# Optimization experiments

Hardware: AMD Instinct MI355X
Metric: run time of the kernel (lower is better)

Reference implementation:

```python
import jax, jax.numpy as jnp
import numpy as np

H = 512
TAU = 5
B = 16384
EPS = 1e-5


def layer_norm(x, gamma, beta):
    mu = jnp.mean(x, axis=-1, keepdims=True)
    var = jnp.var(x, axis=-1, keepdims=True)
    return (x - mu) * jax.lax.rsqrt(var + EPS) * gamma + beta


def setup_inputs() -> dict:
    key = jax.random.key(0)
    ks = jax.random.split(key, 12)
    s = 1.0 / np.sqrt(H)
    inp = {
        "T_t": jax.random.normal(ks[0], (B, H), jnp.float32),
        "S_t": jax.random.normal(ks[1], (B, H), jnp.float32),
        "t_att": jax.random.normal(ks[2], (TAU, B, H), jnp.float32),
        "s_att": jax.random.normal(ks[3], (TAU, B, H), jnp.float32),
        # Lin_t_next: in_features(H) -> H, + LayerNorm
        "W_tn": jax.random.uniform(ks[4], (H, H), jnp.float32, -s, s),
        "b_tn": jnp.zeros((H,), jnp.float32),
        "g_tn": jnp.ones((H,), jnp.float32),
        "be_tn": jnp.zeros((H,), jnp.float32),
        # Lin_s_next: H -> H, + LayerNorm
        "W_sn": jax.random.uniform(ks[5], (H, H), jnp.float32, -s, s),
        "b_sn": jnp.zeros((H,), jnp.float32),
        "g_sn": jnp.ones((H,), jnp.float32),
        "be_sn": jnp.zeros((H,), jnp.float32),
        # Lin_t: H -> 3H, + LayerNorm
        "W_t": jax.random.uniform(ks[6], (H, 3 * H), jnp.float32, -s, s),
        "b_t": jnp.zeros((3 * H,), jnp.float32),
        "g_t": jnp.ones((3 * H,), jnp.float32),
        "be_t": jnp.zeros((3 * H,), jnp.float32),
        # Lin_s: H -> 3H, + LayerNorm
        "W_s": jax.random.uniform(ks[7], (H, 3 * H), jnp.float32, -s, s),
        "b_s": jnp.zeros((3 * H,), jnp.float32),
        "g_s": jnp.ones((3 * H,), jnp.float32),
        "be_s": jnp.zeros((3 * H,), jnp.float32),
    }
    return inp


def reference(T_t, S_t, t_att, s_att,
              W_tn, b_tn, g_tn, be_tn,
              W_sn, b_sn, g_sn, be_sn,
              W_t, b_t, g_t, be_t,
              W_s, b_s, g_s, be_s):
    s_next = layer_norm(S_t @ W_sn + b_sn, g_sn, be_sn)        # [B,H]
    t_next = layer_norm(T_t @ W_tn + b_tn, g_tn, be_tn)        # [B,H]

    # attention weights over tau trend steps
    scale = 1.0 / jnp.sqrt(jnp.asarray(H, T_t.dtype))
    weights = jnp.einsum('tbh,bh->tb', s_att, s_next) * scale   # [tau,B]
    weights = jax.nn.softmax(weights, axis=0)[..., None]        # [tau,B,1]
    T_trend = jnp.sum(t_att * weights, axis=0)                  # [B,H]

    t_att_gate = jax.nn.sigmoid(t_next)
    T_fusion = T_t * t_att_gate + (1.0 - t_att_gate) * T_trend

    T_concat = layer_norm(T_fusion @ W_t + b_t, g_t, be_t)      # [B,3H]
    S_concat = layer_norm(S_t @ W_s + b_s, g_s, be_s)           # [B,3H]
    t_g, t_t, t_s = jnp.split(T_concat, 3, axis=1)
    s_g, s_t, s_s = jnp.split(S_concat, 3, axis=1)

    T_gate = jax.nn.sigmoid(t_g)
    S_gate = jax.nn.sigmoid(s_g)
    T_new = T_gate * t_t + (1.0 - T_gate) * s_t
    S_new = S_gate * s_s + (1.0 - S_gate) * t_s
    S_new = S_new + S_t  # cell_mode == 'residual'
    return (T_new, S_new)
```

## Files before the change

kernel.cpp:

```cpp
#include <hip/hip_runtime.h>

#define Bsz 16384
#define Hd  512
#define TAUn 5
#define EPSv 1e-5f

typedef short bf16x8 __attribute__((ext_vector_type(8)));
typedef float f32x4  __attribute__((ext_vector_type(4)));

__device__ __forceinline__ float bf2f(short s) {
    union { unsigned u; float f; } v;
    v.u = ((unsigned)(unsigned short)s) << 16;
    return v.f;
}
__device__ __forceinline__ short f2bf(float f) {
    union { float f; unsigned u; } v; v.f = f;
    unsigned r = v.u + 0x7fffu + ((v.u >> 16) & 1u);
    return (short)(r >> 16);
}
__device__ __forceinline__ float sigm(float x) {
    return 1.0f / (1.0f + expf(-x));
}

__device__ __forceinline__ void gload16(const void* gsrc, void* lds) {
    __builtin_amdgcn_global_load_lds(
        (const __attribute__((address_space(1))) void*)gsrc,
        (__attribute__((address_space(3))) void*)lds, 16, 0, 0);
}

__device__ __forceinline__ float load1(const void* p, size_t i, int isbf) {
    return isbf ? bf2f(((const short*)p)[i]) : ((const float*)p)[i];
}
__device__ __forceinline__ void load8f(const void* p, size_t off, int isbf, float o[8]) {
    if (isbf) {
        bf16x8 v = *(const bf16x8*)((const short*)p + off);
#pragma unroll
        for (int j = 0; j < 8; ++j) o[j] = bf2f(v[j]);
    } else {
        const float* f = (const float*)p + off;
        float4 a = *(const float4*)f, b = *(const float4*)(f + 4);
        o[0]=a.x; o[1]=a.y; o[2]=a.z; o[3]=a.w; o[4]=b.x; o[5]=b.y; o[6]=b.z; o[7]=b.w;
    }
}
__device__ __forceinline__ bf16x8 load8bf(const void* p, size_t off, int isbf) {
    if (isbf) return *(const bf16x8*)((const short*)p + off);
    const float* f = (const float*)p + off;
    bf16x8 r;
#pragma unroll
    for (int j = 0; j < 8; ++j) r[j] = f2bf(f[j]);
    return r;
}

__global__ void detect_dtype(const void* g_tn, int* flag) {
    if (threadIdx.x == 0 && blockIdx.x == 0)
        *flag = (((const unsigned*)g_tn)[0] == 0x3F803F80u) ? 1 : 0;
}

__global__ void transpose_any(const void* __restrict__ in, short* __restrict__ out,
                              int K, int N, const int* __restrict__ flagp) {
    __shared__ short tile[32][33];
    const int isbf = *flagp;
    int n0 = blockIdx.x * 32, k0 = blockIdx.y * 32;
    int tx = threadIdx.x, ty = threadIdx.y;
    for (int i = ty; i < 32; i += 8) {
        size_t idx = (size_t)(k0 + i) * N + n0 + tx;
        tile[i][tx] = isbf ? ((const short*)in)[idx] : f2bf(((const float*)in)[idx]);
    }
    __syncthreads();
    for (int i = ty; i < 32; i += 8)
        out[(size_t)(n0 + i) * K + k0 + tx] = tile[tx][i];
}

__global__ __launch_bounds__(256) void conv_bf16(const void* __restrict__ in,
                                                 short* __restrict__ out,
                                                 const int* __restrict__ flagp) {
    const int isbf = *flagp;
    size_t i = ((size_t)blockIdx.x * 256 + threadIdx.x) * 8;
    *(bf16x8*)(out + i) = load8bf(in, i, isbf);
}

__global__ __launch_bounds__(256) void pack_weights(const void* __restrict__ in,
                                                    short* __restrict__ out,
                                                    int N, const int* __restrict__ flagp) {
    const int isbf = *flagp;
    const int lane = threadIdx.x & 63;
    const int packet = blockIdx.x * 4 + (threadIdx.x >> 6);
    const int nc = packet >> 4;
    const int kc = packet & 15;
    const int n  = nc * 16 + (lane & 15);
    const int kb = kc * 32 + (lane >> 4) * 8;
    bf16x8 v;
#pragma unroll
    for (int j = 0; j < 8; ++j) {
        size_t idx = (size_t)(kb + j) * N + n;
        v[j] = isbf ? ((const short*)in)[idx] : f2bf(((const float*)in)[idx]);
    }
    *(bf16x8*)(out + (size_t)packet * 512 + lane * 8) = v;
}

__global__ __launch_bounds__(256) void gemm128(
    const short* __restrict__ A, const short* __restrict__ BT,
    short* __restrict__ C, int N)
{
    __shared__ short As[2][128 * 32];
    __shared__ short Bs[2][128 * 32];
    const int tid  = threadIdx.x;
    const int wv   = tid >> 6, lane = tid & 63;
    const int m16  = lane & 15, quad = lane >> 4;
    const int mt = blockIdx.x & 127, nt = blockIdx.x >> 7;
    const int m0 = mt * 128, n0 = nt * 128;
    const int wm = wv >> 1, wn = wv & 1;

    f32x4 acc[16];
#pragma unroll
    for (int i = 0; i < 16; ++i) acc[i] = (f32x4){0.f, 0.f, 0.f, 0.f};

    auto STAGE = [&](int buf, int kc) {
        const int k0 = kc * 32;
#pragma unroll
        for (int o = 0; o < 2; ++o) {
            int g = o * 256 + tid;
            int row = g >> 2, unit = g & 3;
            gload16(A  + (size_t)(m0 + row) * Hd + k0 + unit * 8,
                    (short*)As[buf] + (size_t)(o * 256 + wv * 64) * 8);
            gload16(BT + (size_t)(n0 + row) * Hd + k0 + unit * 8,
                    (short*)Bs[buf] + (size_t)(o * 256 + wv * 64) * 8);
        }
    };

    STAGE(0, 0);
    __syncthreads();
    for (int kc = 0; kc < 16; ++kc) {
        const int cur = kc & 1;
        if (kc < 15) STAGE(cur ^ 1, kc + 1);
        bf16x8 a[4], b[4];
#pragma unroll
        for (int f = 0; f < 4; ++f) {
            a[f] = *(const bf16x8*)&As[cur][(wm * 64 + f * 16 + m16) * 32 + quad * 8];
            b[f] = *(const bf16x8*)&Bs[cur][(wn * 64 + f * 16 + m16) * 32 + quad * 8];
        }
#pragma unroll
        for (int fm = 0; fm < 4; ++fm)
#pragma unroll
            for (int fn = 0; fn < 4; ++fn)
                acc[fm * 4 + fn] = __builtin_amdgcn_mfma_f32_16x16x32_bf16(
                    a[fm], b[fn], acc[fm * 4 + fn], 0, 0, 0);
        __syncthreads();
    }

#pragma unroll
    for (int fm = 0; fm < 4; ++fm)
#pragma unroll
        for (int fn = 0; fn < 4; ++fn) {
            int col = n0 + wn * 64 + fn * 16 + m16;
#pragma unroll
            for (int r = 0; r < 4; ++r) {
                int row = m0 + wm * 64 + fm * 16 + quad * 4 + r;
                C[(size_t)row * N + col] = f2bf(acc[fm * 4 + fn][r]);
            }
        }
}

__global__ __launch_bounds__(256) void kernelA2(
    const short* __restrict__ Cs, const short* __restrict__ Ct,
    const void* __restrict__ T_t, const void* __restrict__ t_att, const void* __restrict__ s_att,
    const void* __restrict__ b_tn, const void* __restrict__ g_tn, const void* __restrict__ be_tn,
    const void* __restrict__ b_sn, const void* __restrict__ g_sn, const void* __restrict__ be_sn,
    short* __restrict__ T_fus, const int* __restrict__ flagp)
{
    __shared__ float xs[16][Hd + 4];
    __shared__ float xt[16][Hd + 4];
    __shared__ float red[4][16][16];
    __shared__ float stat[4][16];
    __shared__ float wts[TAUn][16];

    const int isbf = *flagp;
    const int tid  = threadIdx.x;
    const int wave = tid >> 6;
    const int lane = tid & 63;
    const int row0 = blockIdx.x * 16;

    for (int i = 0; i < 4; ++i) {
        int unit = tid + i * 256;
        int r = unit >> 6, c = (unit & 63) * 8;
        bf16x8 vs8 = *(const bf16x8*)(Cs + (size_t)(row0 + r) * Hd + c);
        bf16x8 vt8 = *(const bf16x8*)(Ct + (size_t)(row0 + r) * Hd + c);
#pragma unroll
        for (int j = 0; j < 8; ++j) {
            xs[r][c + j] = bf2f(vs8[j]) + load1(b_sn, c + j, isbf);
            xt[r][c + j] = bf2f(vt8[j]) + load1(b_tn, c + j, isbf);
        }
    }
    __syncthreads();

    {
        int r = tid >> 4, lw = tid & 15;
        float s1 = 0, s2 = 0, t1 = 0, t2 = 0;
        for (int c = lw; c < Hd; c += 16) {
            float v = xs[r][c]; s1 += v; s2 += v * v;
            float u = xt[r][c]; t1 += u; t2 += u * u;
        }
        red[0][r][lw] = s1; red[1][r][lw] = s2; red[2][r][lw] = t1; red[3][r][lw] = t2;
    }
    __syncthreads();
    if (tid < 16) {
        float a = 0, b = 0, c = 0, d = 0;
        for (int i = 0; i < 16; ++i) { a += red[0][tid][i]; b += red[1][tid][i]; c += red[2][tid][i]; d += red[3][tid][i]; }
        float muS = a / Hd, varS = b / Hd - muS * muS;
        float muT = c / Hd, varT = d / Hd - muT * muT;
        stat[0][tid] = muS; stat[1][tid] = rsqrtf(varS + EPSv);
        stat[2][tid] = muT; stat[3][tid] = rsqrtf(varT + EPSv);
    }
    __syncthreads();
    for (int idx = tid; idx < 16 * Hd; idx += 256) {
        int r = idx >> 9, c = idx & (Hd - 1);
        xs[r][c] = (xs[r][c] - stat[0][r]) * stat[1][r] * load1(g_sn, c, isbf) + load1(be_sn, c, isbf);
        xt[r][c] = (xt[r][c] - stat[2][r]) * stat[3][r] * load1(g_tn, c, isbf) + load1(be_tn, c, isbf);
    }
    __syncthreads();

    const float scale = 0.044194173824159216f;
    for (int r2 = 0; r2 < 4; ++r2) {
        int row = wave * 4 + r2;
        size_t b = (size_t)(row0 + row);
        float xsv[8];
#pragma unroll
        for (int j = 0; j < 8; ++j) xsv[j] = xs[row][lane * 8 + j];
        for (int t = 0; t < TAUn; ++t) {
            float sa[8];
            load8f(s_att, ((size_t)t * Bsz + b) * Hd + lane * 8, isbf, sa);
            float p = 0;
#pragma unroll
            for (int j = 0; j < 8; ++j) p += sa[j] * xsv[j];
            for (int off = 32; off > 0; off >>= 1) p += __shfl_xor(p, off);
            if (lane == 0) wts[t][row] = p * scale;
        }
    }
    __syncthreads();
    if (tid < 16) {
        float mx = -1e30f;
        for (int t = 0; t < TAUn; ++t) mx = fmaxf(mx, wts[t][tid]);
        float e[TAUn], s = 0;
        for (int t = 0; t < TAUn; ++t) { e[t] = expf(wts[t][tid] - mx); s += e[t]; }
        for (int t = 0; t < TAUn; ++t) wts[t][tid] = e[t] / s;
    }
    __syncthreads();

    for (int it = 0; it < 4; ++it) {
        int c = tid + it * 256;
        int row = c >> 6, h0 = (c & 63) * 8;
        size_t b = (size_t)(row0 + row);
        float tt[8];
        load8f(T_t, b * Hd + h0, isbf, tt);
        float w[TAUn];
        for (int t = 0; t < TAUn; ++t) w[t] = wts[t][row];
        float ta[TAUn][8];
        for (int t = 0; t < TAUn; ++t)
            load8f(t_att, ((size_t)t * Bsz + b) * Hd + h0, isbf, ta[t]);
        bf16x8 o;
#pragma unroll
        for (int j = 0; j < 8; ++j) {
            float g = sigm(xt[row][h0 + j]);
            float trend = 0;
            for (int t = 0; t < TAUn; ++t) trend += w[t] * ta[t][j];
            o[j] = f2bf(tt[j] * g + (1.f - g) * trend);
        }
        *(bf16x8*)(T_fus + b * Hd + h0) = o;
    }
}

__global__ __launch_bounds__(256) void kernelC2(
    const short* __restrict__ Cu, const short* __restrict__ Cv, const void* __restrict__ S_t,
    const void* __restrict__ b_t, const void* __restrict__ g_t, const void* __restrict__ be_t,
    const void* __restrict__ b_s, const void* __restrict__ g_s, const void* __restrict__ be_s,
    void* __restrict__ out, const int* __restrict__ flagp)
{
    const int isbf = *flagp;
    const int lane = threadIdx.x & 63;
    const size_t row = (size_t)blockIdx.x * 4 + (threadIdx.x >> 6);
    const float n3inv = 1.0f / 1536.0f;

    float u[3][8], v[3][8];
    float su = 0, qu = 0, sv = 0, qv = 0;
#pragma unroll
    for (int k = 0; k < 3; ++k) {
        int c0 = (k * 64 + lane) * 8;
        bf16x8 a = *(const bf16x8*)(Cu + row * 1536 + c0);
        bf16x8 b = *(const bf16x8*)(Cv + row * 1536 + c0);
        float bt[8], bs[8];
        load8f(b_t, c0, isbf, bt);
        load8f(b_s, c0, isbf, bs);
#pragma unroll
        for (int j = 0; j < 8; ++j) {
            float x = bf2f(a[j]) + bt[j];
            float y = bf2f(b[j]) + bs[j];
            u[k][j] = x; v[k][j] = y;
            su += x; qu += x * x; sv += y; qv += y * y;
        }
    }
    for (int mk = 32; mk >= 1; mk >>= 1) {
        su += __shfl_xor(su, mk); qu += __shfl_xor(qu, mk);
        sv += __shfl_xor(sv, mk); qv += __shfl_xor(qv, mk);
    }
    float muU = su * n3inv, rU = rsqrtf(qu * n3inv - muU * muU + EPSv);
    float muV = sv * n3inv, rV = rsqrtf(qv * n3inv - muV * muV + EPSv);

    float guv[3][8], beu[3][8], gvv[3][8], bev[3][8];
#pragma unroll
    for (int k = 0; k < 3; ++k) {
        int c0 = (k * 64 + lane) * 8;
        load8f(g_t,  c0, isbf, guv[k]);
        load8f(be_t, c0, isbf, beu[k]);
        load8f(g_s,  c0, isbf, gvv[k]);
        load8f(be_s, c0, isbf, bev[k]);
    }
    float stv[8];
    load8f(S_t, row * Hd + lane * 8, isbf, stv);

    float Tn[8], Sn[8];
#pragma unroll
    for (int j = 0; j < 8; ++j) {
        float ug = (u[0][j] - muU) * rU * guv[0][j] + beu[0][j];
        float ut = (u[1][j] - muU) * rU * guv[1][j] + beu[1][j];
        float us = (u[2][j] - muU) * rU * guv[2][j] + beu[2][j];
        float vg = (v[0][j] - muV) * rV * gvv[0][j] + bev[0][j];
        float vt = (v[1][j] - muV) * rV * gvv[1][j] + bev[1][j];
        float vs = (v[2][j] - muV) * rV * gvv[2][j] + bev[2][j];
        float Tg = sigm(ug), Sg = sigm(vg);
        Tn[j] = Tg * ut + (1.f - Tg) * vt;
        Sn[j] = Sg * vs + (1.f - Sg) * us + stv[j];
    }

    size_t o0 = row * Hd + lane * 8;
    size_t o1 = (size_t)Bsz * Hd + o0;
    if (isbf) {
        bf16x8 oT, oS;
#pragma unroll
        for (int j = 0; j < 8; ++j) { oT[j] = f2bf(Tn[j]); oS[j] = f2bf(Sn[j]); }
        *(bf16x8*)((short*)out + o0) = oT;
        *(bf16x8*)((short*)out + o1) = oS;
    } else {
        float* of = (float*)out;
        *(float4*)(of + o0)     = (float4){Tn[0], Tn[1], Tn[2], Tn[3]};
        *(float4*)(of + o0 + 4) = (float4){Tn[4], Tn[5], Tn[6], Tn[7]};
        *(float4*)(of + o1)     = (float4){Sn[0], Sn[1], Sn[2], Sn[3]};
        *(float4*)(of + o1 + 4) = (float4){Sn[4], Sn[5], Sn[6], Sn[7]};
    }
}

__global__ __launch_bounds__(256) void kernelA(
    const void* __restrict__ T_t, const void* __restrict__ S_t,
    const void* __restrict__ t_att, const void* __restrict__ s_att,
    const short* __restrict__ WtnP, const short* __restrict__ WsnP,
    const void* __restrict__ b_tn, const void* __restrict__ g_tn, const void* __restrict__ be_tn,
    const void* __restrict__ b_sn, const void* __restrict__ g_sn, const void* __restrict__ be_sn,
    short* __restrict__ T_fus, const int* __restrict__ flagp)
{
    __shared__ float xs[16][Hd + 4];
    __shared__ float xt[16][Hd + 4];
    __shared__ float red[4][16][16];
    __shared__ float stat[4][16];
    __shared__ float wts[TAUn][16];

    const int isbf = *flagp;
    const int tid  = threadIdx.x;
    const int wave = tid >> 6;
    const int lane = tid & 63;
    const int m16  = lane & 15;
    const int quad = lane >> 4;
    const int row0 = blockIdx.x * 16;

    f32x4 accS[8], accT[8];
#pragma unroll
    for (int i = 0; i < 8; ++i) { accS[i] = (f32x4){0.f,0.f,0.f,0.f}; accT[i] = (f32x4){0.f,0.f,0.f,0.f}; }

    const size_t arow = (size_t)(row0 + m16) * Hd + quad * 8;
    const int nw = wave * 128;

    for (int kc = 0; kc < 16; ++kc) {
        const int k0 = kc * 32;
        bf16x8 aS = load8bf(S_t, arow + k0, isbf);
        bf16x8 aT = load8bf(T_t, arow + k0, isbf);
#pragma unroll
        for (int t = 0; t < 8; ++t) {
            size_t off = (size_t)((((wave * 8 + t) * 16 + kc) * 64) + lane) * 8;
            bf16x8 bS = *(const bf16x8*)(WsnP + off);
            bf16x8 bT = *(const bf16x8*)(WtnP + off);
            accS[t] = __builtin_amdgcn_mfma_f32_16x16x32_bf16(aS, bS, accS[t], 0, 0, 0);
            accT[t] = __builtin_amdgcn_mfma_f32_16x16x32_bf16(aT, bT, accT[t], 0, 0, 0);
        }
    }
#pragma unroll
    for (int t = 0; t < 8; ++t) {
        int col = nw + t * 16 + m16;
        float bs = load1(b_sn, col, isbf), bt = load1(b_tn, col, isbf);
#pragma unroll
        for (int r = 0; r < 4; ++r) {
            xs[quad * 4 + r][col] = accS[t][r] + bs;
            xt[quad * 4 + r][col] = accT[t][r] + bt;
        }
    }
    __syncthreads();

    {
        int r = tid >> 4, lw = tid & 15;
        float s1 = 0, s2 = 0, t1 = 0, t2 = 0;
        for (int c = lw; c < Hd; c += 16) {
            float v = xs[r][c]; s1 += v; s2 += v * v;
            float u = xt[r][c]; t1 += u; t2 += u * u;
        }
        red[0][r][lw] = s1; red[1][r][lw] = s2; red[2][r][lw] = t1; red[3][r][lw] = t2;
    }
    __syncthreads();
    if (tid < 16) {
        float a = 0, b = 0, c = 0, d = 0;
        for (int i = 0; i < 16; ++i) { a += red[0][tid][i]; b += red[1][tid][i]; c += red[2][tid][i]; d += red[3][tid][i]; }
        float muS = a / Hd, varS = b / Hd - muS * muS;
        float muT = c / Hd, varT = d / Hd - muT * muT;
        stat[0][tid] = muS; stat[1][tid] = rsqrtf(varS + EPSv);
        stat[2][tid] = muT; stat[3][tid] = rsqrtf(varT + EPSv);
    }
    __syncthreads();
    for (int idx = tid; idx < 16 * Hd; idx += 256) {
        int r = idx >> 9, c = idx & (Hd - 1);
        xs[r][c] = (xs[r][c] - stat[0][r]) * stat[1][r] * load1(g_sn, c, isbf) + load1(be_sn, c, isbf);
        xt[r][c] = (xt[r][c] - stat[2][r]) * stat[3][r] * load1(g_tn, c, isbf) + load1(be_tn, c, isbf);
    }
    __syncthreads();

    const float scale = 0.044194173824159216f;
    for (int r2 = 0; r2 < 4; ++r2) {
        int row = wave * 4 + r2;
        size_t b = (size_t)(row0 + row);
        float xsv[8];
#pragma unroll
        for (int j = 0; j < 8; ++j) xsv[j] = xs[row][lane * 8 + j];
        for (int t = 0; t < TAUn; ++t) {
            float sa[8];
            load8f(s_att, ((size_t)t * Bsz + b) * Hd + lane * 8, isbf, sa);
            float p = 0;
#pragma unroll
            for (int j = 0; j < 8; ++j) p += sa[j] * xsv[j];
            for (int off = 32; off > 0; off >>= 1) p += __shfl_xor(p, off);
            if (lane == 0) wts[t][row] = p * scale;
        }
    }
    __syncthreads();
    if (tid < 16) {
        float mx = -1e30f;
        for (int t = 0; t < TAUn; ++t) mx = fmaxf(mx, wts[t][tid]);
        float e[TAUn], s = 0;
        for (int t = 0; t < TAUn; ++t) { e[t] = expf(wts[t][tid] - mx); s += e[t]; }
        for (int t = 0; t < TAUn; ++t) wts[t][tid] = e[t] / s;
    }
    __syncthreads();

    for (int it = 0; it < 4; ++it) {
        int c = tid + it * 256;
        int row = c >> 6, h0 = (c & 63) * 8;
        size_t b = (size_t)(row0 + row);
        float tt[8];
        load8f(T_t, b * Hd + h0, isbf, tt);
        float w[TAUn];
        for (int t = 0; t < TAUn; ++t) w[t] = wts[t][row];
        float ta[TAUn][8];
        for (int t = 0; t < TAUn; ++t)
            load8f(t_att, ((size_t)t * Bsz + b) * Hd + h0, isbf, ta[t]);
        bf16x8 o;
#pragma unroll
        for (int j = 0; j < 8; ++j) {
            float g = sigm(xt[row][h0 + j]);
            float trend = 0;
            for (int t = 0; t < TAUn; ++t) trend += w[t] * ta[t][j];
            o[j] = f2bf(tt[j] * g + (1.f - g) * trend);
        }
        *(bf16x8*)(T_fus + b * Hd + h0) = o;
    }
}

__global__ __launch_bounds__(512) void kernelB(
    const short* __restrict__ T_fus, const void* __restrict__ S_t,
    const short* __restrict__ WtP, const short* __restrict__ WsP,
    const void* __restrict__ b_t, const void* __restrict__ g_t, const void* __restrict__ be_t,
    const void* __restrict__ b_s, const void* __restrict__ g_s, const void* __restrict__ be_s,
    void* __restrict__ out, const int* __restrict__ flagp)
{
    __shared__ float red[4][16][8];
    __shared__ float stat[4][16];

    const int isbf = *flagp;
    const int tid  = threadIdx.x;
    const int wave = tid >> 6;
    const int lane = tid & 63;
    const int m16  = lane & 15;
    const int quad = lane >> 4;
    const int row0 = blockIdx.x * 16;
    const int N3 = 3 * Hd;

    f32x4 accU[12], accV[12];
#pragma unroll
    for (int i = 0; i < 12; ++i) { accU[i] = (f32x4){0.f,0.f,0.f,0.f}; accV[i] = (f32x4){0.f,0.f,0.f,0.f}; }

    const short* A1 = T_fus + (size_t)(row0 + m16) * Hd + quad * 8;
    const size_t a2row = (size_t)(row0 + m16) * Hd + quad * 8;

    for (int kc = 0; kc < 16; ++kc) {
        const int k0 = kc * 32;
        bf16x8 a1 = *(const bf16x8*)(A1 + k0);
        bf16x8 a2 = load8bf(S_t, a2row + k0, isbf);
#pragma unroll
        for (int th = 0; th < 3; ++th) {
#pragma unroll
            for (int t = 0; t < 4; ++t) {
                int nc = th * 32 + wave * 4 + t;
                size_t off = (size_t)(((nc * 16 + kc) * 64) + lane) * 8;
                bf16x8 bU = *(const bf16x8*)(WtP + off);
                bf16x8 bV = *(const bf16x8*)(WsP + off);
                accU[th * 4 + t] = __builtin_amdgcn_mfma_f32_16x16x32_bf16(a1, bU, accU[th * 4 + t], 0, 0, 0);
                accV[th * 4 + t] = __builtin_amdgcn_mfma_f32_16x16x32_bf16(a2, bV, accV[th * 4 + t], 0, 0, 0);
            }
        }
    }
#pragma unroll
    for (int i = 0; i < 12; ++i) {
        int th = i >> 2, t = i & 3;
        int col = th * Hd + wave * 64 + t * 16 + m16;
        float bu = load1(b_t, col, isbf), bv = load1(b_s, col, isbf);
#pragma unroll
        for (int r = 0; r < 4; ++r) { accU[i][r] += bu; accV[i][r] += bv; }
    }
    float sU[4] = {0,0,0,0}, qU[4] = {0,0,0,0}, sV[4] = {0,0,0,0}, qV[4] = {0,0,0,0};
#pragma unroll
    for (int i = 0; i < 12; ++i)
#pragma unroll
        for (int r = 0; r < 4; ++r) {
            float u = accU[i][r]; sU[r] += u; qU[r] += u * u;
            float v = accV[i][r]; sV[r] += v; qV[r] += v * v;
        }
    for (int mk = 8; mk >= 1; mk >>= 1)
#pragma unroll
        for (int r = 0; r < 4; ++r) {
            sU[r] += __shfl_xor(sU[r], mk); qU[r] += __shfl_xor(qU[r], mk);
            sV[r] += __shfl_xor(sV[r], mk); qV[r] += __shfl_xor(qV[r], mk);
        }
    if (m16 == 0)
#pragma unroll
        for (int r = 0; r < 4; ++r) {
            int row = quad * 4 + r;
            red[0][row][wave] = sU[r]; red[1][row][wave] = qU[r];
            red[2][row][wave] = sV[r]; red[3][row][wave] = qV[r];
        }
    __syncthreads();
    if (tid < 16) {
        float a = 0, b = 0, c = 0, d = 0;
        for (int w = 0; w < 8; ++w) { a += red[0][tid][w]; b += red[1][tid][w]; c += red[2][tid][w]; d += red[3][tid][w]; }
        float muU = a / N3, varU = b / N3 - muU * muU;
        float muV = c / N3, varV = d / N3 - muV * muV;
        stat[0][tid] = muU; stat[1][tid] = rsqrtf(varU + EPSv);
        stat[2][tid] = muV; stat[3][tid] = rsqrtf(varV + EPSv);
    }
    __syncthreads();

    short* out_b = (short*)out;
    float* out_f = (float*)out;
#pragma unroll
    for (int t = 0; t < 4; ++t) {
        int c = wave * 64 + t * 16 + m16;
        float gt0 = load1(g_t, c, isbf),        bt0 = load1(be_t, c, isbf);
        float gt1 = load1(g_t, c + 512, isbf),  bt1 = load1(be_t, c + 512, isbf);
        float gt2 = load1(g_t, c + 1024, isbf), bt2 = load1(be_t, c + 1024, isbf);
        float gs0 = load1(g_s, c, isbf),        bs0 = load1(be_s, c, isbf);
        float gs1 = load1(g_s, c + 512, isbf),  bs1 = load1(be_s, c + 512, isbf);
        float gs2 = load1(g_s, c + 1024, isbf), bs2 = load1(be_s, c + 1024, isbf);
#pragma unroll
        for (int r = 0; r < 4; ++r) {
            int row = quad * 4 + r;
            size_t grow = (size_t)(row0 + row);
            float mU = stat[0][row], rU = stat[1][row];
            float mV = stat[2][row], rV = stat[3][row];
            float ug = (accU[t][r]     - mU) * rU * gt0 + bt0;
            float ut = (accU[4 + t][r] - mU) * rU * gt1 + bt1;
            float us = (accU[8 + t][r] - mU) * rU * gt2 + bt2;
            float vg = (accV[t][r]     - mV) * rV * gs0 + bs0;
            float vt = (accV[4 + t][r] - mV) * rV * gs1 + bs1;
            float vs = (accV[8 + t][r] - mV) * rV * gs2 + bs2;
            float Tg = sigm(ug), Sg = sigm(vg);
            float Tn = Tg * ut + (1.f - Tg) * vt;
            float Sn = Sg * vs + (1.f - Sg) * us + load1(S_t, grow * Hd + c, isbf);
            size_t i0 = grow * Hd + c;
            size_t i1 = (size_t)Bsz * Hd + grow * Hd + c;
            if (isbf) { out_b[i0] = f2bf(Tn); out_b[i1] = f2bf(Sn); }
            else      { out_f[i0] = Tn;       out_f[i1] = Sn; }
        }
    }
}

extern "C" void kernel_launch(void* const* d_in, const int* in_sizes, int n_in,
                              void* d_out, int out_size, void* d_ws, size_t ws_size,
                              hipStream_t stream) {
    const void* T_t   = d_in[0];
    const void* S_t   = d_in[1];
    const void* t_att = d_in[2];
    const void* s_att = d_in[3];
    const void* W_tn  = d_in[4];
    const void* b_tn  = d_in[5];
    const void* g_tn  = d_in[6];
    const void* be_tn = d_in[7];
    const void* W_sn  = d_in[8];
    const void* b_sn  = d_in[9];
    const void* g_sn  = d_in[10];
    const void* be_sn = d_in[11];
    const void* W_t   = d_in[12];
    const void* b_t   = d_in[13];
    const void* g_t   = d_in[14];
    const void* be_t  = d_in[15];
    const void* W_s   = d_in[16];
    const void* b_s   = d_in[17];
    const void* g_s   = d_in[18];
    const void* be_s  = d_in[19];

    int*   flag = (int*)d_ws;
    short* p    = (short*)d_ws + 8;
    short* WtnP = p; p += 512 * 512;
    short* WsnP = p; p += 512 * 512;
    short* Tfus = p; p += (size_t)Bsz * 512;
    short* WtP  = p; p += (size_t)512 * 1536;
    short* WsP  = p; p += (size_t)512 * 1536;
    short* WtnT = p; p += 512 * 512;
    short* WsnT = p; p += 512 * 512;
    short* WtT  = p; p += (size_t)512 * 1536;
    short* WsT  = p; p += (size_t)512 * 1536;
    short* S_bf = p; p += (size_t)Bsz * 512;
    short* T_bf = p; p += (size_t)Bsz * 512;
    short* Cu   = p; p += (size_t)Bsz * 1536;
    short* Cv   = p; p += (size_t)Bsz * 1536;
    size_t need = (size_t)((char*)p - (char*)d_ws);

    detect_dtype<<<1, 64, 0, stream>>>(g_tn, flag);
    dim3 tb(32, 8);

    if (ws_size >= need) {
        transpose_any<<<dim3(16, 16), tb, 0, stream>>>(W_tn, WtnT, 512, 512, flag);
        transpose_any<<<dim3(16, 16), tb, 0, stream>>>(W_sn, WsnT, 512, 512, flag);
        transpose_any<<<dim3(48, 16), tb, 0, stream>>>(W_t,  WtT,  512, 1536, flag);
        transpose_any<<<dim3(48, 16), tb, 0, stream>>>(W_s,  WsT,  512, 1536, flag);
        conv_bf16<<<4096, 256, 0, stream>>>(S_t, S_bf, flag);
        conv_bf16<<<4096, 256, 0, stream>>>(T_t, T_bf, flag);

        gemm128<<<4 * 128, 256, 0, stream>>>(S_bf, WsnT, Cu, 512);
        gemm128<<<4 * 128, 256, 0, stream>>>(T_bf, WtnT, Cv, 512);
        kernelA2<<<Bsz / 16, 256, 0, stream>>>(Cu, Cv, T_t, t_att, s_att,
                                               b_tn, g_tn, be_tn, b_sn, g_sn, be_sn, Tfus, flag);

        gemm128<<<12 * 128, 256, 0, stream>>>(Tfus, WtT, Cu, 1536);
        gemm128<<<12 * 128, 256, 0, stream>>>(S_bf, WsT, Cv, 1536);
        kernelC2<<<Bsz / 4, 256, 0, stream>>>(Cu, Cv, S_t,
                                              b_t, g_t, be_t, b_s, g_s, be_s, d_out, flag);
    } else {
        pack_weights<<<dim3((32 * 16) / 4), 256, 0, stream>>>(W_tn, WtnP, 512, flag);
        pack_weights<<<dim3((32 * 16) / 4), 256, 0, stream>>>(W_sn, WsnP, 512, flag);
        pack_weights<<<dim3((96 * 16) / 4), 256, 0, stream>>>(W_t,  WtP,  1536, flag);
        pack_weights<<<dim3((96 * 16) / 4), 256, 0, stream>>>(W_s,  WsP,  1536, flag);
        kernelA<<<Bsz / 16, 256, 0, stream>>>(T_t, S_t, t_att, s_att, WtnP, WsnP,
                                              b_tn, g_tn, be_tn, b_sn, g_sn, be_sn, Tfus, flag);
        kernelB<<<Bsz / 16, 512, 0, stream>>>(Tfus, S_t, WtP, WsP,
                                              b_t, g_t, be_t, b_s, g_s, be_s, d_out, flag);
    }
}
```

Measured before the change: 700.2 us.

## Make kernelA2 one-wave-per-row with shuffle reductions; skip bf16 conversion when inputs are bf16

Rewrites the LayerNorm/attention/fusion kernel so each 64-lane wave owns one row and keeps the row in registers. LayerNorm statistics and the attention dot products are reduced with wave shuffles, which removes the shared-memory staging and the several block-wide barriers. Grid size grows from Bsz/16 to Bsz/4 blocks. Separately, when the host-side input size shows S_t/T_t are already bf16, the two conversion kernels are skipped and the raw inputs feed the GEMMs directly.

```diff
diff --git a/kernel.cpp b/kernel.cpp
--- a/kernel.cpp
+++ b/kernel.cpp
@@ -168,105 +168,78 @@
     const void* __restrict__ b_sn, const void* __restrict__ g_sn, const void* __restrict__ be_sn,
     short* __restrict__ T_fus, const int* __restrict__ flagp)
 {
-    __shared__ float xs[16][Hd + 4];
-    __shared__ float xt[16][Hd + 4];
-    __shared__ float red[4][16][16];
-    __shared__ float stat[4][16];
-    __shared__ float wts[TAUn][16];
-
     const int isbf = *flagp;
-    const int tid  = threadIdx.x;
-    const int wave = tid >> 6;
-    const int lane = tid & 63;
-    const int row0 = blockIdx.x * 16;
-
-    for (int i = 0; i < 4; ++i) {
-        int unit = tid + i * 256;
-        int r = unit >> 6, c = (unit & 63) * 8;
-        bf16x8 vs8 = *(const bf16x8*)(Cs + (size_t)(row0 + r) * Hd + c);
-        bf16x8 vt8 = *(const bf16x8*)(Ct + (size_t)(row0 + r) * Hd + c);
-#pragma unroll
-        for (int j = 0; j < 8; ++j) {
-            xs[r][c + j] = bf2f(vs8[j]) + load1(b_sn, c + j, isbf);
-            xt[r][c + j] = bf2f(vt8[j]) + load1(b_tn, c + j, isbf);
-        }
-    }
-    __syncthreads();
-
-    {
-        int r = tid >> 4, lw = tid & 15;
-        float s1 = 0, s2 = 0, t1 = 0, t2 = 0;
-        for (int c = lw; c < Hd; c += 16) {
-            float v = xs[r][c]; s1 += v; s2 += v * v;
-            float u = xt[r][c]; t1 += u; t2 += u * u;
-        }
-        red[0][r][lw] = s1; red[1][r][lw] = s2; red[2][r][lw] = t1; red[3][r][lw] = t2;
-    }
-    __syncthreads();
-    if (tid < 16) {
-        float a = 0, b = 0, c = 0, d = 0;
-        for (int i = 0; i < 16; ++i) { a += red[0][tid][i]; b += red[1][tid][i]; c += red[2][tid][i]; d += red[3][tid][i]; }
-        float muS = a / Hd, varS = b / Hd - muS * muS;
-        float muT = c / Hd, varT = d / Hd - muT * muT;
-        stat[0][tid] = muS; stat[1][tid] = rsqrtf(varS + EPSv);
-        stat[2][tid] = muT; stat[3][tid] = rsqrtf(varT + EPSv);
-    }
-    __syncthreads();
-    for (int idx = tid; idx < 16 * Hd; idx += 256) {
-        int r = idx >> 9, c = idx & (Hd - 1);
-        xs[r][c] = (xs[r][c] - stat[0][r]) * stat[1][r] * load1(g_sn, c, isbf) + load1(be_sn, c, isbf);
-        xt[r][c] = (xt[r][c] - stat[2][r]) * stat[3][r] * load1(g_tn, c, isbf) + load1(be_tn, c, isbf);
-    }
-    __syncthreads();
+    const int lane = threadIdx.x & 63;
+    const size_t row = (size_t)blockIdx.x * 4 + (threadIdx.x >> 6);
+    const int c0 = lane * 8;
+    const float hinv = 1.0f / 512.0f;
+
+    bf16x8 cs8 = *(const bf16x8*)(Cs + row * Hd + c0);
+    bf16x8 ct8 = *(const bf16x8*)(Ct + row * Hd + c0);
+    float bs[8], btn[8];
+    load8f(b_sn, c0, isbf, bs);
+    load8f(b_tn, c0, isbf, btn);
+    float xs[8], xt[8];
+    float s1 = 0, s2 = 0, t1 = 0, t2 = 0;
+#pragma unroll
+    for (int j = 0; j < 8; ++j) {
+        float x = bf2f(cs8[j]) + bs[j];
+        float y = bf2f(ct8[j]) + btn[j];
+        xs[j] = x; xt[j] = y;
+        s1 += x; s2 += x * x; t1 += y; t2 += y * y;
+    }
+    for (int mk = 32; mk >= 1; mk >>= 1) {
+        s1 += __shfl_xor(s1, mk); s2 += __shfl_xor(s2, mk);
+        t1 += __shfl_xor(t1, mk); t2 += __shfl_xor(t2, mk);
+    }
+    float muS = s1 * hinv, rS = rsqrtf(s2 * hinv - muS * muS + EPSv);
+    float muT = t1 * hinv, rT = rsqrtf(t2 * hinv - muT * muT + EPSv);
+
+    float gs[8], bes[8], gtv[8], bet[8];
+    load8f(g_sn,  c0, isbf, gs);
+    load8f(be_sn, c0, isbf, bes);
+    load8f(g_tn,  c0, isbf, gtv);
+    load8f(be_tn, c0, isbf, bet);
+#pragma unroll
+    for (int j = 0; j < 8; ++j) {
+        xs[j] = (xs[j] - muS) * rS * gs[j] + bes[j];
+        xt[j] = (xt[j] - muT) * rT * gtv[j] + bet[j];
+    }
 
     const float scale = 0.044194173824159216f;
-    for (int r2 = 0; r2 < 4; ++r2) {
-        int row = wave * 4 + r2;
-        size_t b = (size_t)(row0 + row);
-        float xsv[8];
-#pragma unroll
-        for (int j = 0; j < 8; ++j) xsv[j] = xs[row][lane * 8 + j];
-        for (int t = 0; t < TAUn; ++t) {
-            float sa[8];
-            load8f(s_att, ((size_t)t * Bsz + b) * Hd + lane * 8, isbf, sa);
-            float p = 0;
-#pragma unroll
-            for (int j = 0; j < 8; ++j) p += sa[j] * xsv[j];
-            for (int off = 32; off > 0; off >>= 1) p += __shfl_xor(p, off);
-            if (lane == 0) wts[t][row] = p * scale;
-        }
-    }
-    __syncthreads();
-    if (tid < 16) {
-        float mx = -1e30f;
-        for (int t = 0; t < TAUn; ++t) mx = fmaxf(mx, wts[t][tid]);
-        float e[TAUn], s = 0;
-        for (int t = 0; t < TAUn; ++t) { e[t] = expf(wts[t][tid] - mx); s += e[t]; }
-        for (int t = 0; t < TAUn; ++t) wts[t][tid] = e[t] / s;
-    }
-    __syncthreads();
-
-    for (int it = 0; it < 4; ++it) {
-        int c = tid + it * 256;
-        int row = c >> 6, h0 = (c & 63) * 8;
-        size_t b = (size_t)(row0 + row);
-        float tt[8];
-        load8f(T_t, b * Hd + h0, isbf, tt);
-        float w[TAUn];
-        for (int t = 0; t < TAUn; ++t) w[t] = wts[t][row];
-        float ta[TAUn][8];
-        for (int t = 0; t < TAUn; ++t)
-            load8f(t_att, ((size_t)t * Bsz + b) * Hd + h0, isbf, ta[t]);
-        bf16x8 o;
-#pragma unroll
-        for (int j = 0; j < 8; ++j) {
-            float g = sigm(xt[row][h0 + j]);
-            float trend = 0;
-            for (int t = 0; t < TAUn; ++t) trend += w[t] * ta[t][j];
-            o[j] = f2bf(tt[j] * g + (1.f - g) * trend);
-        }
-        *(bf16x8*)(T_fus + b * Hd + h0) = o;
-    }
+    float w[TAUn];
+    for (int t = 0; t < TAUn; ++t) {
+        float sa[8];
+        load8f(s_att, ((size_t)t * Bsz + row) * Hd + c0, isbf, sa);
+        float p = 0;
+#pragma unroll
+        for (int j = 0; j < 8; ++j) p += sa[j] * xs[j];
+        for (int mk = 32; mk >= 1; mk >>= 1) p += __shfl_xor(p, mk);
+        w[t] = p * scale;
+    }
+    float mx = -1e30f;
+    for (int t = 0; t < TAUn; ++t) mx = fmaxf(mx, w[t]);
+    float ssum = 0;
+    for (int t = 0; t < TAUn; ++t) { w[t] = expf(w[t] - mx); ssum += w[t]; }
+    float sinv = 1.0f / ssum;
+    for (int t = 0; t < TAUn; ++t) w[t] *= sinv;
+
+    float tt[8];
+    load8f(T_t, row * Hd + c0, isbf, tt);
+    float trend[8] = {0, 0, 0, 0, 0, 0, 0, 0};
+    for (int t = 0; t < TAUn; ++t) {
+        float ta[8];
+        load8f(t_att, ((size_t)t * Bsz + row) * Hd + c0, isbf, ta);
+#pragma unroll
+        for (int j = 0; j < 8; ++j) trend[j] += w[t] * ta[j];
+    }
+    bf16x8 o;
+#pragma unroll
+    for (int j = 0; j < 8; ++j) {
+        float g = sigm(xt[j]);
+        o[j] = f2bf(tt[j] * g + (1.f - g) * trend[j]);
+    }
+    *(bf16x8*)(T_fus + row * Hd + c0) = o;
 }
 
 __global__ __launch_bounds__(256) void kernelC2(
@@ -644,16 +617,22 @@
         transpose_any<<<dim3(16, 16), tb, 0, stream>>>(W_sn, WsnT, 512, 512, flag);
         transpose_any<<<dim3(48, 16), tb, 0, stream>>>(W_t,  WtT,  512, 1536, flag);
         transpose_any<<<dim3(48, 16), tb, 0, stream>>>(W_s,  WsT,  512, 1536, flag);
-        conv_bf16<<<4096, 256, 0, stream>>>(S_t, S_bf, flag);
-        conv_bf16<<<4096, 256, 0, stream>>>(T_t, T_bf, flag);
-
-        gemm128<<<4 * 128, 256, 0, stream>>>(S_bf, WsnT, Cu, 512);
-        gemm128<<<4 * 128, 256, 0, stream>>>(T_bf, WtnT, Cv, 512);
-        kernelA2<<<Bsz / 16, 256, 0, stream>>>(Cu, Cv, T_t, t_att, s_att,
-                                               b_tn, g_tn, be_tn, b_sn, g_sn, be_sn, Tfus, flag);
+
+        const int bf_host = (in_sizes && in_sizes[0] == (int)((size_t)Bsz * Hd * 2)) ? 1 : 0;
+        const short* As = bf_host ? (const short*)S_t : S_bf;
+        const short* At = bf_host ? (const short*)T_t : T_bf;
+        if (!bf_host) {
+            conv_bf16<<<4096, 256, 0, stream>>>(S_t, S_bf, flag);
+            conv_bf16<<<4096, 256, 0, stream>>>(T_t, T_bf, flag);
+        }
+
+        gemm128<<<4 * 128, 256, 0, stream>>>(As, WsnT, Cu, 512);
+        gemm128<<<4 * 128, 256, 0, stream>>>(At, WtnT, Cv, 512);
+        kernelA2<<<Bsz / 4, 256, 0, stream>>>(Cu, Cv, T_t, t_att, s_att,
+                                              b_tn, g_tn, be_tn, b_sn, g_sn, be_sn, Tfus, flag);
 
         gemm128<<<12 * 128, 256, 0, stream>>>(Tfus, WtT, Cu, 1536);
-        gemm128<<<12 * 128, 256, 0, stream>>>(S_bf, WsT, Cv, 1536);
+        gemm128<<<12 * 128, 256, 0, stream>>>(As, WsT, Cv, 1536);
         kernelC2<<<Bsz / 4, 256, 0, stream>>>(Cu, Cv, S_t,
                                               b_t, g_t, be_t, b_s, g_s, be_s, d_out, flag);
     } else {
```

Result: faster. 656.0 us (-6.3%).
